# Performance work log

Hardware: AMD Instinct MI355X
Metric: run time of the kernel (lower is better)

The kernel has to match this reference:

```python
import jax, jax.numpy as jnp
import numpy as np

N_NODES = 10000
N_EDGES = 160000
T_STEPS = 2
N_SAMPLE = 2
H_DIM = 64
Z_DIM = 32
K_HEADS = 4
N_IN = 4


def setup_inputs() -> dict:
    key = jax.random.key(0)
    ks = jax.random.split(key, 16)
    sc = lambda fan_in: 1.0 / np.sqrt(fan_in).astype(np.float32)
    inp = {}
    inp["inputs"] = jax.random.normal(ks[0], (N_NODES, T_STEPS, N_IN), jnp.float32)
    inp["zA"] = jax.random.normal(ks[1], (N_NODES, N_SAMPLE, Z_DIM), jnp.float32)
    inp["zG"] = jax.random.normal(ks[2], (N_NODES, N_SAMPLE, Z_DIM), jnp.float32)
    inp["src"] = jax.random.randint(ks[3], (N_EDGES,), 0, N_NODES)
    inp["dst"] = jax.random.randint(ks[4], (N_EDGES,), 0, N_NODES)
    # GAT attention projections (K heads, no bias): Linear(z_dim -> h_dim)
    inp["Ws"] = jax.random.normal(ks[5], (K_HEADS, H_DIM, Z_DIM), jnp.float32) * sc(Z_DIM)
    inp["Wd"] = jax.random.normal(ks[6], (K_HEADS, H_DIM, Z_DIM), jnp.float32) * sc(Z_DIM)
    # F2: Linear(2h -> h, no bias), ReLU, Linear(h -> h, no bias)
    inp["F2_w1"] = jax.random.normal(ks[7], (H_DIM, 2 * H_DIM), jnp.float32) * sc(2 * H_DIM)
    inp["F2_w2"] = jax.random.normal(ks[8], (H_DIM, H_DIM), jnp.float32) * sc(H_DIM)
    # F1: Linear(K*h -> h, no bias), ReLU, Linear(h -> h, no bias)
    inp["F1_w1"] = jax.random.normal(ks[9], (H_DIM, K_HEADS * H_DIM), jnp.float32) * sc(K_HEADS * H_DIM)
    inp["F1_w2"] = jax.random.normal(ks[10], (H_DIM, H_DIM), jnp.float32) * sc(H_DIM)
    # x_enc: Linear(n_in -> h) with bias
    inp["xenc_w"] = jax.random.normal(ks[11], (H_DIM, N_IN), jnp.float32) * sc(N_IN)
    inp["xenc_b"] = jnp.zeros((H_DIM,), jnp.float32)
    # out_fc: Linear(h+z -> h), ReLU, Linear(h -> 4)
    inp["out_w1"] = jax.random.normal(ks[12], (H_DIM, H_DIM + Z_DIM), jnp.float32) * sc(H_DIM + Z_DIM)
    inp["out_b1"] = jnp.zeros((H_DIM,), jnp.float32)
    inp["out_w2"] = jax.random.normal(ks[13], (4, H_DIM), jnp.float32) * sc(H_DIM)
    inp["out_b2"] = jnp.zeros((4,), jnp.float32)
    inp["pred_steps"] = 2
    return inp


def reference(inputs, zA, zG, src, dst, Ws, Wd, F2_w1, F2_w2, F1_w1, F1_w2,
              xenc_w, xenc_b, out_w1, out_b1, out_w2, out_b2, pred_steps):
    N, T, _ = inputs.shape
    S = zA.shape[1]
    K = Ws.shape[0]

    # --- edge attention (GAT.attn), computed once per forward ---
    As = jnp.einsum('nsz,khz->nskh', zG, Ws)          # [N, S, K, H]
    Ad = jnp.einsum('nsz,khz->nskh', zG, Wd)
    e = jnp.sum(As[src] * Ad[dst], axis=-1)           # [E, S, K]
    e = jax.nn.leaky_relu(e, 0.01)
    # per-destination softmax over incoming edges (DGL mailbox softmax over dim=1)
    m = jax.ops.segment_max(e, dst, num_segments=N)
    ex = jnp.exp(e - m[dst])
    denom = jax.ops.segment_sum(ex, dst, num_segments=N)
    alpha = ex / denom[dst]                           # [E, S, K]
    deg = jax.ops.segment_sum(jnp.ones((e.shape[0],), e.dtype), dst, num_segments=N)
    deg = jnp.maximum(deg, 1.0)[:, None, None]        # [N, 1, 1]; mean over mailbox dim

    def step(xt):
        xt_enc = xt @ xenc_w.T + xenc_b               # [N, S, H]
        cat = jnp.concatenate([xt_enc[src], xt_enc[dst]], axis=-1)  # [E, S, 2H]
        dA = jax.nn.relu(cat @ F2_w1.T) @ F2_w2.T     # [E, S, H]
        # per-head attention-weighted mean over in-neighbors; loop over K (small, fixed)
        res = [jax.ops.segment_sum(alpha[:, :, k:k + 1] * dA, dst, num_segments=N) / deg
               for k in range(K)]
        res = jnp.concatenate(res, axis=-1)           # [N, S, K*H]
        deltax = jax.nn.relu(res @ F1_w1.T) @ F1_w2.T # [N, S, H]
        h = jnp.concatenate([deltax, zA], axis=-1)    # [N, S, H+Z]
        dx = jax.nn.relu(h @ out_w1.T + out_b1) @ out_w2.T + out_b2  # [N, S, 4]
        return xt + dx

    inp_t = jnp.transpose(inputs, (1, 0, 2))          # [T, N, n_in]
    inp_t = jnp.broadcast_to(inp_t[:, :, None, :], (T, N, S, inp_t.shape[-1]))
    preds = []
    for b in range(0, T, pred_steps):                 # blocks of pred_steps
        xt = inp_t[b]
        for _ in range(pred_steps):
            xt = step(xt)
            preds.append(xt)
    out = jnp.stack(preds, axis=0)                    # [T, N, S, 4]
    return jnp.transpose(out, (1, 0, 2, 3))           # [N, T, S, 4]
```

## Files before the change

### kernel.cpp

```cpp
#include <hip/hip_runtime.h>

#define NN 10000
#define NE 160000
#define TT 2
#define SS 2
#define HH 64
#define ZZ 32
#define KK 4
#define NIN 4

typedef short bf16x8 __attribute__((ext_vector_type(8)));
typedef float f32x4 __attribute__((ext_vector_type(4)));

__device__ __forceinline__ unsigned short f2b(float x) {
    unsigned u = __float_as_uint(x);
    u += 0x7fffu + ((u >> 16) & 1u);
    return (unsigned short)(u >> 16);
}
__device__ __forceinline__ float bf2f(unsigned short u) {
    return __uint_as_float(((unsigned)u) << 16);
}

__global__ void k_attnM(const float* __restrict__ Ws, const float* __restrict__ Wd,
                        float* __restrict__ MT) {
    int k = blockIdx.x >> 5;
    int i = blockIdx.x & 31;
    int j = threadIdx.x;
    float acc = 0.0f;
    for (int h = 0; h < HH; ++h)
        acc += Ws[(k*HH + h)*ZZ + i] * Wd[(k*HH + h)*ZZ + j];
    MT[(k*ZZ + j)*ZZ + i] = acc;
}

__global__ void k_qd(const float* __restrict__ zG, const float* __restrict__ MT,
                     unsigned short* __restrict__ qdb) {
    int t = blockIdx.x * blockDim.x + threadIdx.x;
    if (t >= NN*SS*KK*ZZ) return;
    int i  = t & 31;
    int k  = (t >> 5) & 3;
    int ns = t >> 7;
    const float* zg = zG + ns*ZZ;
    const float* mt = MT + k*ZZ*ZZ;
    float acc = 0.0f;
#pragma unroll
    for (int j = 0; j < ZZ; ++j) acc += mt[j*ZZ + i] * zg[j];
    qdb[t] = f2b(acc);
}

__global__ void k_fold(const float* __restrict__ F2w1, const float* __restrict__ xw,
                       const float* __restrict__ xb,
                       float* __restrict__ G1, float* __restrict__ G2,
                       float* __restrict__ c1, float* __restrict__ c2) {
    int t = threadIdx.x;
    int h = t >> 2, i = t & 3;
    float a1 = 0.f, a2 = 0.f;
    for (int j = 0; j < HH; ++j) {
        float x = xw[j*NIN + i];
        a1 += F2w1[h*128 + j] * x;
        a2 += F2w1[h*128 + 64 + j] * x;
    }
    G1[h*4 + i] = a1;
    G2[h*4 + i] = a2;
    if (i == 0) {
        float b1 = 0.f, b2 = 0.f;
        for (int j = 0; j < HH; ++j) {
            float bb = xb[j];
            b1 += F2w1[h*128 + j] * bb;
            b2 += F2w1[h*128 + 64 + j] * bb;
        }
        c1[h] = b1; c2[h] = b2;
    }
}

__global__ void k_init(const float* __restrict__ inputs, float* __restrict__ xt,
                       const int* __restrict__ dst, int* __restrict__ deg_i) {
    int t = blockIdx.x * blockDim.x + threadIdx.x;
    if (t < NE) atomicAdd(deg_i + dst[t], 1);
    if (t < NN*SS*NIN) {
        int i = t & 3;
        int n = t >> 3;
        xt[t] = inputs[n*(TT*NIN) + i];
    }
}

__global__ void k_scan(const int* __restrict__ deg_i, int* __restrict__ offsets,
                       int* __restrict__ cursor) {
    __shared__ int buf0[1024], buf1[1024];
    int tidx = threadIdx.x;
    const int CH = (NN + 1023) / 1024;
    int b0 = tidx * CH;
    int sum = 0;
    for (int i = 0; i < CH; ++i) { int idx = b0 + i; if (idx < NN) sum += deg_i[idx]; }
    buf0[tidx] = sum;
    __syncthreads();
    int* s = buf0; int* d = buf1;
    for (int off = 1; off < 1024; off <<= 1) {
        d[tidx] = s[tidx] + (tidx >= off ? s[tidx - off] : 0);
        __syncthreads();
        int* tmp = s; s = d; d = tmp;
    }
    int run = s[tidx] - sum;
    for (int i = 0; i < CH; ++i) {
        int idx = b0 + i;
        if (idx < NN) { offsets[idx] = run; cursor[idx] = run; run += deg_i[idx]; }
    }
    if (tidx == 0) offsets[NN] = NE;
}

__global__ void k_scatter(const int* __restrict__ src, const int* __restrict__ dst,
                          int* __restrict__ cursor, int* __restrict__ src_by_pos,
                          int* __restrict__ dst_by_pos) {
    int e = blockIdx.x * blockDim.x + threadIdx.x;
    if (e >= NE) return;
    int sn = src[e], dn = dst[e];
    int pos = atomicAdd(cursor + dn, 1);
    src_by_pos[pos] = sn;
    dst_by_pos[pos] = dn;
}

__global__ __launch_bounds__(256) void k_edge_e(
    const unsigned short* __restrict__ qdb, const unsigned short* __restrict__ zGb,
    const int* __restrict__ src_by_pos, const int* __restrict__ dst_by_pos,
    float* __restrict__ e_csr) {
    int t = blockIdx.x * blockDim.x + threadIdx.x;
    if (t >= NE*SS) return;
    int s = t & 1;
    int idx = t >> 1;
    int sn = src_by_pos[idx], dn = dst_by_pos[idx];
    const unsigned* zp = (const unsigned*)(zGb + (sn*SS + s)*ZZ);
    float zf[32];
#pragma unroll
    for (int j = 0; j < 16; ++j) {
        unsigned u = zp[j];
        zf[2*j]   = __uint_as_float(u << 16);
        zf[2*j+1] = __uint_as_float(u & 0xffff0000u);
    }
    const unsigned* qp = (const unsigned*)(qdb + (dn*SS + s)*KK*ZZ);
    float ev[4];
#pragma unroll
    for (int k = 0; k < 4; ++k) {
        float a = 0.f;
#pragma unroll
        for (int j = 0; j < 16; ++j) {
            unsigned u = qp[k*16 + j];
            a += __uint_as_float(u << 16) * zf[2*j]
               + __uint_as_float(u & 0xffff0000u) * zf[2*j+1];
        }
        ev[k] = a > 0.f ? a : 0.01f*a;
    }
    *(float4*)(e_csr + t*4) = *(float4*)ev;
}

__global__ __launch_bounds__(64) void k_salpha(
    const float* __restrict__ e_csr, const int* __restrict__ offsets,
    float* __restrict__ alpha) {
    int item = blockIdx.x;
    int n = item >> 1, s = item & 1;
    int l = threadIdx.x;
    int i = l >> 2, k = l & 3;
    int r0 = offsets[n], r1 = offsets[n+1];
    float mx = -1e30f;
    for (int idx = r0 + i; idx < r1; idx += 16)
        mx = fmaxf(mx, e_csr[(idx*2 + s)*4 + k]);
#pragma unroll
    for (int off = 4; off < 64; off <<= 1) mx = fmaxf(mx, __shfl_xor(mx, off));
    float sum = 0.f;
    for (int idx = r0 + i; idx < r1; idx += 16)
        sum += __expf(e_csr[(idx*2 + s)*4 + k] - mx);
#pragma unroll
    for (int off = 4; off < 64; off <<= 1) sum += __shfl_xor(sum, off);
    int deg = r1 - r0;
    float dd = (float)(deg > 1 ? deg : 1);
    float inv = sum > 0.f ? 1.f/(sum*dd) : 0.f;
    for (int idx = r0 + i; idx < r1; idx += 16)
        alpha[(idx*2 + s)*4 + k] = __expf(e_csr[(idx*2 + s)*4 + k] - mx) * inv;
}

__global__ void k_conv_all(const float* __restrict__ F2w2,
                           const float* __restrict__ F1w1, const float* __restrict__ F1w2,
                           const float* __restrict__ ow1, const float* __restrict__ ow2,
                           const float* __restrict__ zA, const float* __restrict__ zG,
                           unsigned short* __restrict__ W2b,
                           unsigned short* __restrict__ F1w1b, unsigned short* __restrict__ F1w2b,
                           unsigned short* __restrict__ ow1b, unsigned short* __restrict__ ow2b,
                           unsigned short* __restrict__ zAb, unsigned short* __restrict__ zGb) {
    int t = blockIdx.x * blockDim.x + threadIdx.x;
    if (t < NN*SS*ZZ) { zAb[t] = f2b(zA[t]); zGb[t] = f2b(zG[t]); }
    if (t < HH*HH)    { W2b[t] = f2b(F2w2[t]); F1w2b[t] = f2b(F1w2[t]); }
    if (t < HH*KK*HH) F1w1b[t] = f2b(F1w1[t]);
    if (t < HH*(HH+ZZ)) ow1b[t] = f2b(ow1[t]);
    if (t < 4*HH)     ow2b[t] = f2b(ow2[t]);
}

__global__ __launch_bounds__(64) void k_agg2(
    const float* __restrict__ xt, const float* __restrict__ G1,
    const float* __restrict__ G2, const float* __restrict__ c1,
    const float* __restrict__ c2, const int* __restrict__ src_by_pos,
    const int* __restrict__ offsets, const float* __restrict__ alpha,
    unsigned short* __restrict__ agg_b)
{
    int item = blockIdx.x;
    int n = item >> 1, s = item & 1;
    int h = threadIdx.x;
    int r0 = offsets[n], r1 = offsets[n+1];
    const float4 g1 = *(const float4*)(G1 + h*4);
    const float4 g2 = *(const float4*)(G2 + h*4);
    const float4 xd = *(const float4*)(xt + item*4);
    float p2 = c2[h] + xd.x*g2.x + xd.y*g2.y + xd.z*g2.z + xd.w*g2.w;
    float c1h = c1[h];
    float a0 = 0.f, a1 = 0.f, a2 = 0.f, a3 = 0.f;
    int idx = r0;
    for (; idx + 4 <= r1; idx += 4) {
        int sn0 = src_by_pos[idx];
        int sn1 = src_by_pos[idx+1];
        int sn2 = src_by_pos[idx+2];
        int sn3 = src_by_pos[idx+3];
        float4 x0 = *(const float4*)(xt + (sn0*SS + s)*NIN);
        float4 x1 = *(const float4*)(xt + (sn1*SS + s)*NIN);
        float4 x2 = *(const float4*)(xt + (sn2*SS + s)*NIN);
        float4 x3 = *(const float4*)(xt + (sn3*SS + s)*NIN);
        float4 w0 = *(const float4*)(alpha + ((idx+0)*2 + s)*4);
        float4 w1 = *(const float4*)(alpha + ((idx+1)*2 + s)*4);
        float4 w2 = *(const float4*)(alpha + ((idx+2)*2 + s)*4);
        float4 w3 = *(const float4*)(alpha + ((idx+3)*2 + s)*4);
        float p, hd;
        p = c1h + x0.x*g1.x + x0.y*g1.y + x0.z*g1.z + x0.w*g1.w;
        hd = p + p2; hd = hd > 0.f ? hd : 0.f;
        a0 += w0.x*hd; a1 += w0.y*hd; a2 += w0.z*hd; a3 += w0.w*hd;
        p = c1h + x1.x*g1.x + x1.y*g1.y + x1.z*g1.z + x1.w*g1.w;
        hd = p + p2; hd = hd > 0.f ? hd : 0.f;
        a0 += w1.x*hd; a1 += w1.y*hd; a2 += w1.z*hd; a3 += w1.w*hd;
        p = c1h + x2.x*g1.x + x2.y*g1.y + x2.z*g1.z + x2.w*g1.w;
        hd = p + p2; hd = hd > 0.f ? hd : 0.f;
        a0 += w2.x*hd; a1 += w2.y*hd; a2 += w2.z*hd; a3 += w2.w*hd;
        p = c1h + x3.x*g1.x + x3.y*g1.y + x3.z*g1.z + x3.w*g1.w;
        hd = p + p2; hd = hd > 0.f ? hd : 0.f;
        a0 += w3.x*hd; a1 += w3.y*hd; a2 += w3.z*hd; a3 += w3.w*hd;
    }
    for (; idx < r1; ++idx) {
        int sn = src_by_pos[idx];
        float4 x0 = *(const float4*)(xt + (sn*SS + s)*NIN);
        float4 w0 = *(const float4*)(alpha + (idx*2 + s)*4);
        float p = c1h + x0.x*g1.x + x0.y*g1.y + x0.z*g1.z + x0.w*g1.w;
        float hd = p + p2; hd = hd > 0.f ? hd : 0.f;
        a0 += w0.x*hd; a1 += w0.y*hd; a2 += w0.z*hd; a3 += w0.w*hd;
    }
    agg_b[item*256 +       h] = f2b(a0);
    agg_b[item*256 + 64  + h] = f2b(a1);
    agg_b[item*256 + 128 + h] = f2b(a2);
    agg_b[item*256 + 192 + h] = f2b(a3);
}

__global__ __launch_bounds__(256) void k_node_mfma(
    const unsigned short* __restrict__ agg_b, const unsigned short* __restrict__ zAb,
    const unsigned short* __restrict__ W2b,
    const unsigned short* __restrict__ F1w1b, const unsigned short* __restrict__ F1w2b,
    const unsigned short* __restrict__ ow1b, const unsigned short* __restrict__ ow2b,
    const float* __restrict__ ob1, const float* __restrict__ ob2,
    float* __restrict__ xt, float* __restrict__ out, int tstep)
{
    __shared__ unsigned short res_s[4][16*264];
    __shared__ unsigned short hid_s[4][16*72];
    __shared__ unsigned short hcat_s[4][16*104];
    int tid = threadIdx.x;
    int w = tid >> 6, l = tid & 63, l15 = l & 15, qq = l >> 4;

    bf16x8 w2f[2][4], b2f[2][4], o1f[3][4], bo2[2];
#pragma unroll
    for (int nb = 0; nb < 4; ++nb) {
        int n = nb*16 + l15;
#pragma unroll
        for (int kb = 0; kb < 2; ++kb) {
            w2f[kb][nb] = *(const bf16x8*)(W2b  + n*64 + kb*32 + qq*8);
            b2f[kb][nb] = *(const bf16x8*)(F1w2b + n*64 + kb*32 + qq*8);
        }
#pragma unroll
        for (int kb = 0; kb < 3; ++kb)
            o1f[kb][nb] = *(const bf16x8*)(ow1b + n*96 + kb*32 + qq*8);
    }
#pragma unroll
    for (int kb = 0; kb < 2; ++kb) {
        if (l15 < 4) bo2[kb] = *(const bf16x8*)(ow2b + l15*64 + kb*32 + qq*8);
        else {
            bf16x8 z;
#pragma unroll
            for (int j = 0; j < 8; ++j) z[j] = 0;
            bo2[kb] = z;
        }
    }
    float b1v[4];
#pragma unroll
    for (int nb = 0; nb < 4; ++nb) b1v[nb] = ob1[nb*16 + l15];
    float b2v = (l15 < 4) ? ob2[l15] : 0.0f;

    int itemBase = blockIdx.x*64 + w*16;
    if (itemBase >= NN*SS) return;

    *(uint4*)(&hcat_s[w][l15*104 + 64 + qq*8]) =
        *(const uint4*)(zAb + (itemBase + l15)*ZZ + qq*8);

#pragma unroll
    for (int k = 0; k < 4; ++k) {
        f32x4 acc0[4];
#pragma unroll
        for (int nb = 0; nb < 4; ++nb) acc0[nb] = (f32x4)(0.0f);
#pragma unroll
        for (int kb = 0; kb < 2; ++kb) {
            bf16x8 af = *(const bf16x8*)(agg_b + (itemBase + l15)*256 + k*64 + kb*32 + qq*8);
#pragma unroll
            for (int nb = 0; nb < 4; ++nb)
                acc0[nb] = __builtin_amdgcn_mfma_f32_16x16x32_bf16(af, w2f[kb][nb], acc0[nb], 0, 0, 0);
        }
#pragma unroll
        for (int nb = 0; nb < 4; ++nb)
#pragma unroll
            for (int r = 0; r < 4; ++r)
                res_s[w][(qq*4 + r)*264 + k*64 + nb*16 + l15] = f2b(acc0[nb][r]);
    }

    f32x4 acc[4];
#pragma unroll
    for (int nb = 0; nb < 4; ++nb) acc[nb] = (f32x4)(0.0f);
#pragma unroll
    for (int kb = 0; kb < 8; ++kb) {
        bf16x8 af = *(const bf16x8*)(&res_s[w][l15*264 + kb*32 + qq*8]);
#pragma unroll
        for (int nb = 0; nb < 4; ++nb) {
            bf16x8 bf = *(const bf16x8*)(F1w1b + (nb*16 + l15)*256 + kb*32 + qq*8);
            acc[nb] = __builtin_amdgcn_mfma_f32_16x16x32_bf16(af, bf, acc[nb], 0, 0, 0);
        }
    }
#pragma unroll
    for (int nb = 0; nb < 4; ++nb)
#pragma unroll
        for (int r = 0; r < 4; ++r) {
            float v = acc[nb][r];
            hid_s[w][(qq*4 + r)*72 + nb*16 + l15] = f2b(v > 0.0f ? v : 0.0f);
        }

    f32x4 acc2[4];
#pragma unroll
    for (int nb = 0; nb < 4; ++nb) acc2[nb] = (f32x4)(0.0f);
#pragma unroll
    for (int kb = 0; kb < 2; ++kb) {
        bf16x8 af = *(const bf16x8*)(&hid_s[w][l15*72 + kb*32 + qq*8]);
#pragma unroll
        for (int nb = 0; nb < 4; ++nb)
            acc2[nb] = __builtin_amdgcn_mfma_f32_16x16x32_bf16(af, b2f[kb][nb], acc2[nb], 0, 0, 0);
    }
#pragma unroll
    for (int nb = 0; nb < 4; ++nb)
#pragma unroll
        for (int r = 0; r < 4; ++r)
            hcat_s[w][(qq*4 + r)*104 + nb*16 + l15] = f2b(acc2[nb][r]);

    f32x4 acc3[4];
#pragma unroll
    for (int nb = 0; nb < 4; ++nb) acc3[nb] = (f32x4)(0.0f);
#pragma unroll
    for (int kb = 0; kb < 3; ++kb) {
        bf16x8 af = *(const bf16x8*)(&hcat_s[w][l15*104 + kb*32 + qq*8]);
#pragma unroll
        for (int nb = 0; nb < 4; ++nb)
            acc3[nb] = __builtin_amdgcn_mfma_f32_16x16x32_bf16(af, o1f[kb][nb], acc3[nb], 0, 0, 0);
    }
#pragma unroll
    for (int nb = 0; nb < 4; ++nb)
#pragma unroll
        for (int r = 0; r < 4; ++r) {
            float v = acc3[nb][r] + b1v[nb];
            hid_s[w][(qq*4 + r)*72 + nb*16 + l15] = f2b(v > 0.0f ? v : 0.0f);
        }

    f32x4 acc4 = (f32x4)(0.0f);
#pragma unroll
    for (int kb = 0; kb < 2; ++kb) {
        bf16x8 af = *(const bf16x8*)(&hid_s[w][l15*72 + kb*32 + qq*8]);
        acc4 = __builtin_amdgcn_mfma_f32_16x16x32_bf16(af, bo2[kb], acc4, 0, 0, 0);
    }
    if (l15 < 4) {
#pragma unroll
        for (int r = 0; r < 4; ++r) {
            int item = itemBase + qq*4 + r;
            float nx = xt[item*4 + l15] + acc4[r] + b2v;
            xt[item*4 + l15] = nx;
            int n = item >> 1, s = item & 1;
            out[((n*TT + tstep)*SS + s)*4 + l15] = nx;
        }
    }
}

extern "C" void kernel_launch(void* const* d_in, const int* in_sizes, int n_in,
                              void* d_out, int out_size, void* d_ws, size_t ws_size,
                              hipStream_t stream) {
    const float* inputs = (const float*)d_in[0];
    const float* zA     = (const float*)d_in[1];
    const float* zG     = (const float*)d_in[2];
    const int*   src    = (const int*)d_in[3];
    const int*   dst    = (const int*)d_in[4];
    const float* Ws     = (const float*)d_in[5];
    const float* Wd     = (const float*)d_in[6];
    const float* F2w1   = (const float*)d_in[7];
    const float* F2w2   = (const float*)d_in[8];
    const float* F1w1   = (const float*)d_in[9];
    const float* F1w2   = (const float*)d_in[10];
    const float* xw     = (const float*)d_in[11];
    const float* xb     = (const float*)d_in[12];
    const float* ow1    = (const float*)d_in[13];
    const float* ob1    = (const float*)d_in[14];
    const float* ow2    = (const float*)d_in[15];
    const float* ob2    = (const float*)d_in[16];
    float* out = (float*)d_out;

    float*          base        = (float*)d_ws;
    float*          MT          = base;
    float*          e_csr       = base + 4096;
    float*          alpha       = base + 1284096;
    int*            deg_i       = (int*)(base + 2564096);
    int*            offsets     = (int*)(base + 2574096);
    int*            cursor      = (int*)(base + 2584112);
    int*            src_by_pos  = (int*)(base + 2594112);
    int*            dst_by_pos  = (int*)(base + 2754112);
    float*          xt          = base + 2914112;
    float*          G1f         = base + 2994112;
    float*          G2f         = base + 2994368;
    float*          c1f         = base + 2994624;
    float*          c2f         = base + 2994688;
    unsigned short* W2b         = (unsigned short*)(base + 2994816);
    unsigned short* F1w1b       = (unsigned short*)(base + 2996864);
    unsigned short* F1w2b       = (unsigned short*)(base + 3005056);
    unsigned short* ow1b        = (unsigned short*)(base + 3007104);
    unsigned short* ow2b        = (unsigned short*)(base + 3010176);
    unsigned short* zAb         = (unsigned short*)(base + 3010304);
    unsigned short* zGb         = (unsigned short*)(base + 3330304);
    unsigned short* agg_b       = (unsigned short*)(base + 3650304);
    unsigned short* qdb         = (unsigned short*)(base + 6210304);

    hipMemsetAsync(deg_i, 0, 10000u * 4u, stream);

    k_attnM<<<KK*ZZ, ZZ, 0, stream>>>(Ws, Wd, MT);
    k_qd<<<(NN*SS*KK*ZZ + 255)/256, 256, 0, stream>>>(zG, MT, qdb);
    k_fold<<<1, 256, 0, stream>>>(F2w1, xw, xb, G1f, G2f, c1f, c2f);
    k_conv_all<<<(NN*SS*ZZ + 255)/256, 256, 0, stream>>>(F2w2, F1w1, F1w2, ow1, ow2,
                                                         zA, zG, W2b, F1w1b, F1w2b,
                                                         ow1b, ow2b, zAb, zGb);
    k_init<<<(NE + 255)/256, 256, 0, stream>>>(inputs, xt, dst, deg_i);
    k_scan<<<1, 1024, 0, stream>>>(deg_i, offsets, cursor);
    k_scatter<<<(NE + 255)/256, 256, 0, stream>>>(src, dst, cursor, src_by_pos, dst_by_pos);
    k_edge_e<<<(NE*SS + 255)/256, 256, 0, stream>>>(qdb, zGb, src_by_pos, dst_by_pos, e_csr);
    k_salpha<<<NN*SS, 64, 0, stream>>>(e_csr, offsets, alpha);

    for (int t = 0; t < 2; ++t) {
        k_agg2<<<NN*SS, 64, 0, stream>>>(xt, G1f, G2f, c1f, c2f,
                                         src_by_pos, offsets, alpha, agg_b);
        k_node_mfma<<<(NN*SS + 63)/64, 256, 0, stream>>>(agg_b, zAb, W2b, F1w1b, F1w2b,
                                                         ow1b, ow2b, ob1, ob2, xt, out, t);
    }
}
```

Measured before the change: 266.1 us.

## Fuse setup kernels and compute edge scores inside per-node softmax

Merges the weight-folding, attention-matrix, bf16 conversion, init and degree-count kernels into one launch. It also removes the separate edge-score kernel and its e_csr buffer: the softmax kernel now computes scores directly from the destination's query and the gathered source zG, caching up to eight scores per lane in registers. This cuts launch count and the global round trip for the scores. In exchange, edges beyond eight per lane have their scores recomputed in each softmax pass, and the dst_by_pos array is dropped.

```diff
diff --git a/kernel.cpp b/kernel.cpp
--- a/kernel.cpp
+++ b/kernel.cpp
@@ -21,15 +21,76 @@
     return __uint_as_float(((unsigned)u) << 16);
 }
 
-__global__ void k_attnM(const float* __restrict__ Ws, const float* __restrict__ Wd,
-                        float* __restrict__ MT) {
-    int k = blockIdx.x >> 5;
-    int i = blockIdx.x & 31;
-    int j = threadIdx.x;
-    float acc = 0.0f;
-    for (int h = 0; h < HH; ++h)
-        acc += Ws[(k*HH + h)*ZZ + i] * Wd[(k*HH + h)*ZZ + j];
-    MT[(k*ZZ + j)*ZZ + i] = acc;
+__device__ __forceinline__ float edge_score(const unsigned* __restrict__ zp,
+                                            const float* __restrict__ qf) {
+    float a = 0.f;
+#pragma unroll
+    for (int j = 0; j < 16; ++j) {
+        unsigned u = zp[j];
+        a += __uint_as_float(u << 16) * qf[2*j]
+           + __uint_as_float(u & 0xffff0000u) * qf[2*j+1];
+    }
+    return a > 0.f ? a : 0.01f*a;
+}
+
+__global__ __launch_bounds__(256) void k_prep(
+    const float* __restrict__ Ws, const float* __restrict__ Wd,
+    const float* __restrict__ F2w1, const float* __restrict__ xw,
+    const float* __restrict__ xb, const float* __restrict__ F2w2,
+    const float* __restrict__ F1w1, const float* __restrict__ F1w2,
+    const float* __restrict__ ow1, const float* __restrict__ ow2,
+    const float* __restrict__ zA, const float* __restrict__ zG,
+    const float* __restrict__ inputs, const int* __restrict__ dst,
+    float* __restrict__ MT, float* __restrict__ G1, float* __restrict__ G2,
+    float* __restrict__ c1, float* __restrict__ c2,
+    unsigned short* __restrict__ W2b, unsigned short* __restrict__ F1w1b,
+    unsigned short* __restrict__ F1w2b, unsigned short* __restrict__ ow1b,
+    unsigned short* __restrict__ ow2b, unsigned short* __restrict__ zAb,
+    unsigned short* __restrict__ zGb, float* __restrict__ xt,
+    int* __restrict__ deg_i)
+{
+    int b = blockIdx.x;
+    int tid = threadIdx.x;
+    if (b < 16) {
+        int o = b*256 + tid;
+        int j = o & 31, i = (o >> 5) & 31, k = o >> 10;
+        float acc = 0.0f;
+        for (int h = 0; h < HH; ++h)
+            acc += Ws[(k*HH + h)*ZZ + i] * Wd[(k*HH + h)*ZZ + j];
+        MT[(k*ZZ + j)*ZZ + i] = acc;
+    } else if (b == 16) {
+        int h = tid >> 2, i = tid & 3;
+        float a1 = 0.f, a2 = 0.f;
+        for (int j = 0; j < HH; ++j) {
+            float x = xw[j*NIN + i];
+            a1 += F2w1[h*128 + j] * x;
+            a2 += F2w1[h*128 + 64 + j] * x;
+        }
+        G1[h*4 + i] = a1;
+        G2[h*4 + i] = a2;
+        if (i == 0) {
+            float b1 = 0.f, b2 = 0.f;
+            for (int j = 0; j < HH; ++j) {
+                float bb = xb[j];
+                b1 += F2w1[h*128 + j] * bb;
+                b2 += F2w1[h*128 + 64 + j] * bb;
+            }
+            c1[h] = b1; c2[h] = b2;
+        }
+    } else {
+        int t = (b - 17)*256 + tid;
+        if (t < NN*SS*ZZ) { zAb[t] = f2b(zA[t]); zGb[t] = f2b(zG[t]); }
+        if (t < HH*HH)    { W2b[t] = f2b(F2w2[t]); F1w2b[t] = f2b(F1w2[t]); }
+        if (t < HH*KK*HH) F1w1b[t] = f2b(F1w1[t]);
+        if (t < HH*(HH+ZZ)) ow1b[t] = f2b(ow1[t]);
+        if (t < 4*HH)     ow2b[t] = f2b(ow2[t]);
+        if (t < NN*SS*NIN) {
+            int i = t & 3;
+            int n = t >> 3;
+            xt[t] = inputs[n*(TT*NIN) + i];
+        }
+        if (t < NE) atomicAdd(deg_i + dst[t], 1);
+    }
 }
 
 __global__ void k_qd(const float* __restrict__ zG, const float* __restrict__ MT,
@@ -45,42 +106,6 @@
 #pragma unroll
     for (int j = 0; j < ZZ; ++j) acc += mt[j*ZZ + i] * zg[j];
     qdb[t] = f2b(acc);
-}
-
-__global__ void k_fold(const float* __restrict__ F2w1, const float* __restrict__ xw,
-                       const float* __restrict__ xb,
-                       float* __restrict__ G1, float* __restrict__ G2,
-                       float* __restrict__ c1, float* __restrict__ c2) {
-    int t = threadIdx.x;
-    int h = t >> 2, i = t & 3;
-    float a1 = 0.f, a2 = 0.f;
-    for (int j = 0; j < HH; ++j) {
-        float x = xw[j*NIN + i];
-        a1 += F2w1[h*128 + j] * x;
-        a2 += F2w1[h*128 + 64 + j] * x;
-    }
-    G1[h*4 + i] = a1;
-    G2[h*4 + i] = a2;
-    if (i == 0) {
-        float b1 = 0.f, b2 = 0.f;
-        for (int j = 0; j < HH; ++j) {
-            float bb = xb[j];
-            b1 += F2w1[h*128 + j] * bb;
-            b2 += F2w1[h*128 + 64 + j] * bb;
-        }
-        c1[h] = b1; c2[h] = b2;
-    }
-}
-
-__global__ void k_init(const float* __restrict__ inputs, float* __restrict__ xt,
-                       const int* __restrict__ dst, int* __restrict__ deg_i) {
-    int t = blockIdx.x * blockDim.x + threadIdx.x;
-    if (t < NE) atomicAdd(deg_i + dst[t], 1);
-    if (t < NN*SS*NIN) {
-        int i = t & 3;
-        int n = t >> 3;
-        xt[t] = inputs[n*(TT*NIN) + i];
-    }
 }
 
 __global__ void k_scan(const int* __restrict__ deg_i, int* __restrict__ offsets,
@@ -108,88 +133,60 @@
 }
 
 __global__ void k_scatter(const int* __restrict__ src, const int* __restrict__ dst,
-                          int* __restrict__ cursor, int* __restrict__ src_by_pos,
-                          int* __restrict__ dst_by_pos) {
+                          int* __restrict__ cursor, int* __restrict__ src_by_pos) {
     int e = blockIdx.x * blockDim.x + threadIdx.x;
     if (e >= NE) return;
-    int sn = src[e], dn = dst[e];
-    int pos = atomicAdd(cursor + dn, 1);
-    src_by_pos[pos] = sn;
-    dst_by_pos[pos] = dn;
-}
-
-__global__ __launch_bounds__(256) void k_edge_e(
+    int pos = atomicAdd(cursor + dst[e], 1);
+    src_by_pos[pos] = src[e];
+}
+
+__global__ __launch_bounds__(64) void k_attn_alpha(
     const unsigned short* __restrict__ qdb, const unsigned short* __restrict__ zGb,
-    const int* __restrict__ src_by_pos, const int* __restrict__ dst_by_pos,
-    float* __restrict__ e_csr) {
-    int t = blockIdx.x * blockDim.x + threadIdx.x;
-    if (t >= NE*SS) return;
-    int s = t & 1;
-    int idx = t >> 1;
-    int sn = src_by_pos[idx], dn = dst_by_pos[idx];
-    const unsigned* zp = (const unsigned*)(zGb + (sn*SS + s)*ZZ);
-    float zf[32];
-#pragma unroll
-    for (int j = 0; j < 16; ++j) {
-        unsigned u = zp[j];
-        zf[2*j]   = __uint_as_float(u << 16);
-        zf[2*j+1] = __uint_as_float(u & 0xffff0000u);
-    }
-    const unsigned* qp = (const unsigned*)(qdb + (dn*SS + s)*KK*ZZ);
-    float ev[4];
-#pragma unroll
-    for (int k = 0; k < 4; ++k) {
-        float a = 0.f;
-#pragma unroll
-        for (int j = 0; j < 16; ++j) {
-            unsigned u = qp[k*16 + j];
-            a += __uint_as_float(u << 16) * zf[2*j]
-               + __uint_as_float(u & 0xffff0000u) * zf[2*j+1];
-        }
-        ev[k] = a > 0.f ? a : 0.01f*a;
-    }
-    *(float4*)(e_csr + t*4) = *(float4*)ev;
-}
-
-__global__ __launch_bounds__(64) void k_salpha(
-    const float* __restrict__ e_csr, const int* __restrict__ offsets,
-    float* __restrict__ alpha) {
+    const int* __restrict__ src_by_pos, const int* __restrict__ offsets,
+    float* __restrict__ alpha)
+{
     int item = blockIdx.x;
     int n = item >> 1, s = item & 1;
     int l = threadIdx.x;
     int i = l >> 2, k = l & 3;
     int r0 = offsets[n], r1 = offsets[n+1];
+    float qf[32];
+    const unsigned* qp = (const unsigned*)(qdb + (item*KK + k)*ZZ);
+#pragma unroll
+    for (int j = 0; j < 16; ++j) {
+        unsigned u = qp[j];
+        qf[2*j]   = __uint_as_float(u << 16);
+        qf[2*j+1] = __uint_as_float(u & 0xffff0000u);
+    }
+    float E[8];
     float mx = -1e30f;
-    for (int idx = r0 + i; idx < r1; idx += 16)
-        mx = fmaxf(mx, e_csr[(idx*2 + s)*4 + k]);
+    int nit = 0;
+    for (int idx = r0 + i; idx < r1; idx += 16, ++nit) {
+        int sn = src_by_pos[idx];
+        float e = edge_score((const unsigned*)(zGb + (sn*SS + s)*ZZ), qf);
+        if (nit < 8) E[nit] = e;
+        mx = fmaxf(mx, e);
+    }
 #pragma unroll
     for (int off = 4; off < 64; off <<= 1) mx = fmaxf(mx, __shfl_xor(mx, off));
     float sum = 0.f;
-    for (int idx = r0 + i; idx < r1; idx += 16)
-        sum += __expf(e_csr[(idx*2 + s)*4 + k] - mx);
+    nit = 0;
+    for (int idx = r0 + i; idx < r1; idx += 16, ++nit) {
+        float e = (nit < 8) ? E[nit]
+                : edge_score((const unsigned*)(zGb + (src_by_pos[idx]*SS + s)*ZZ), qf);
+        sum += __expf(e - mx);
+    }
 #pragma unroll
     for (int off = 4; off < 64; off <<= 1) sum += __shfl_xor(sum, off);
     int deg = r1 - r0;
     float dd = (float)(deg > 1 ? deg : 1);
     float inv = sum > 0.f ? 1.f/(sum*dd) : 0.f;
-    for (int idx = r0 + i; idx < r1; idx += 16)
-        alpha[(idx*2 + s)*4 + k] = __expf(e_csr[(idx*2 + s)*4 + k] - mx) * inv;
-}
-
-__global__ void k_conv_all(const float* __restrict__ F2w2,
-                           const float* __restrict__ F1w1, const float* __restrict__ F1w2,
-                           const float* __restrict__ ow1, const float* __restrict__ ow2,
-                           const float* __restrict__ zA, const float* __restrict__ zG,
-                           unsigned short* __restrict__ W2b,
-                           unsigned short* __restrict__ F1w1b, unsigned short* __restrict__ F1w2b,
-                           unsigned short* __restrict__ ow1b, unsigned short* __restrict__ ow2b,
-                           unsigned short* __restrict__ zAb, unsigned short* __restrict__ zGb) {
-    int t = blockIdx.x * blockDim.x + threadIdx.x;
-    if (t < NN*SS*ZZ) { zAb[t] = f2b(zA[t]); zGb[t] = f2b(zG[t]); }
-    if (t < HH*HH)    { W2b[t] = f2b(F2w2[t]); F1w2b[t] = f2b(F1w2[t]); }
-    if (t < HH*KK*HH) F1w1b[t] = f2b(F1w1[t]);
-    if (t < HH*(HH+ZZ)) ow1b[t] = f2b(ow1[t]);
-    if (t < 4*HH)     ow2b[t] = f2b(ow2[t]);
+    nit = 0;
+    for (int idx = r0 + i; idx < r1; idx += 16, ++nit) {
+        float e = (nit < 8) ? E[nit]
+                : edge_score((const unsigned*)(zGb + (src_by_pos[idx]*SS + s)*ZZ), qf);
+        alpha[(idx*2 + s)*4 + k] = __expf(e - mx) * inv;
+    }
 }
 
 __global__ __launch_bounds__(64) void k_agg2(
@@ -414,41 +411,38 @@
 
     float*          base        = (float*)d_ws;
     float*          MT          = base;
-    float*          e_csr       = base + 4096;
-    float*          alpha       = base + 1284096;
-    int*            deg_i       = (int*)(base + 2564096);
-    int*            offsets     = (int*)(base + 2574096);
-    int*            cursor      = (int*)(base + 2584112);
-    int*            src_by_pos  = (int*)(base + 2594112);
-    int*            dst_by_pos  = (int*)(base + 2754112);
-    float*          xt          = base + 2914112;
-    float*          G1f         = base + 2994112;
-    float*          G2f         = base + 2994368;
-    float*          c1f         = base + 2994624;
-    float*          c2f         = base + 2994688;
-    unsigned short* W2b         = (unsigned short*)(base + 2994816);
-    unsigned short* F1w1b       = (unsigned short*)(base + 2996864);
-    unsigned short* F1w2b       = (unsigned short*)(base + 3005056);
-    unsigned short* ow1b        = (unsigned short*)(base + 3007104);
-    unsigned short* ow2b        = (unsigned short*)(base + 3010176);
-    unsigned short* zAb         = (unsigned short*)(base + 3010304);
-    unsigned short* zGb         = (unsigned short*)(base + 3330304);
-    unsigned short* agg_b       = (unsigned short*)(base + 3650304);
-    unsigned short* qdb         = (unsigned short*)(base + 6210304);
+    float*          alpha       = base + 4096;
+    int*            deg_i       = (int*)(base + 1284096);
+    int*            offsets     = (int*)(base + 1294096);
+    int*            cursor      = (int*)(base + 1304112);
+    int*            src_by_pos  = (int*)(base + 1314112);
+    float*          xt          = base + 1474112;
+    float*          G1f         = base + 1554112;
+    float*          G2f         = base + 1554368;
+    float*          c1f         = base + 1554624;
+    float*          c2f         = base + 1554688;
+    unsigned short* W2b         = (unsigned short*)(base + 1554816);
+    unsigned short* F1w1b       = (unsigned short*)(base + 1556864);
+    unsigned short* F1w2b       = (unsigned short*)(base + 1565056);
+    unsigned short* ow1b        = (unsigned short*)(base + 1567104);
+    unsigned short* ow2b        = (unsigned short*)(base + 1570176);
+    unsigned short* zAb         = (unsigned short*)(base + 1570304);
+    unsigned short* zGb         = (unsigned short*)(base + 1890304);
+    unsigned short* agg_b       = (unsigned short*)(base + 2210304);
+    unsigned short* qdb         = (unsigned short*)(base + 4770304);
 
     hipMemsetAsync(deg_i, 0, 10000u * 4u, stream);
 
-    k_attnM<<<KK*ZZ, ZZ, 0, stream>>>(Ws, Wd, MT);
+    const int CONVB = (NN*SS*ZZ + 255)/256;
+    k_prep<<<17 + CONVB, 256, 0, stream>>>(Ws, Wd, F2w1, xw, xb, F2w2, F1w1, F1w2,
+                                           ow1, ow2, zA, zG, inputs, dst,
+                                           MT, G1f, G2f, c1f, c2f,
+                                           W2b, F1w1b, F1w2b, ow1b, ow2b,
+                                           zAb, zGb, xt, deg_i);
     k_qd<<<(NN*SS*KK*ZZ + 255)/256, 256, 0, stream>>>(zG, MT, qdb);
-    k_fold<<<1, 256, 0, stream>>>(F2w1, xw, xb, G1f, G2f, c1f, c2f);
-    k_conv_all<<<(NN*SS*ZZ + 255)/256, 256, 0, stream>>>(F2w2, F1w1, F1w2, ow1, ow2,
-                                                         zA, zG, W2b, F1w1b, F1w2b,
-                                                         ow1b, ow2b, zAb, zGb);
-    k_init<<<(NE + 255)/256, 256, 0, stream>>>(inputs, xt, dst, deg_i);
     k_scan<<<1, 1024, 0, stream>>>(deg_i, offsets, cursor);
-    k_scatter<<<(NE + 255)/256, 256, 0, stream>>>(src, dst, cursor, src_by_pos, dst_by_pos);
-    k_edge_e<<<(NE*SS + 255)/256, 256, 0, stream>>>(qdb, zGb, src_by_pos, dst_by_pos, e_csr);
-    k_salpha<<<NN*SS, 64, 0, stream>>>(e_csr, offsets, alpha);
+    k_scatter<<<(NE + 255)/256, 256, 0, stream>>>(src, dst, cursor, src_by_pos);
+    k_attn_alpha<<<NN*SS, 64, 0, stream>>>(qdb, zGb, src_by_pos, offsets, alpha);
 
     for (int t = 0; t < 2; ++t) {
         k_agg2<<<NN*SS, 64, 0, stream>>>(xt, G1f, G2f, c1f, c2f,
```

Result: faster. 251.1 us (-5.6%).
